# Performance work log

Measured on AMD Instinct MI355X. Metric: run time of the kernel, lower is better.

Reference implementation:

```python
import jax, jax.numpy as jnp
from jax import lax
import numpy as np

B, S = 128, 512
TARGET_SIZE = 32
T = TARGET_SIZE + 4  # tag_size, START = T-2, END = T-1


def setup_inputs() -> dict:
    key = jax.random.key(0)
    k1, k2, k3, k4 = jax.random.split(key, 4)
    feats = jax.random.normal(k1, (B, S, T), dtype=jnp.float32)
    # contiguous-prefix mask (lengths in [S//2, S])
    lengths = jax.random.randint(k2, (B,), S // 2, S + 1)
    mask = (jnp.arange(S)[None, :] < lengths[:, None]).astype(jnp.int32)
    tags = jax.random.randint(k3, (B, S), 0, TARGET_SIZE).astype(jnp.int32)
    # learned transitions, with the hard constraints from __init__
    transitions = 0.1 * jax.random.normal(k4, (T, T), dtype=jnp.float32)
    transitions = transitions.at[:, T - 2].set(-1000.0)  # nothing -> START
    transitions = transitions.at[T - 1, :].set(-1000.0)  # END -> nothing
    return {"feats": feats, "transitions": transitions, "mask": mask, "tags": tags}


def _nll(feats, transitions, mask, tags):
    # feats: (B,S,T), transitions: (T,T) with [i,j] = score(prev=i -> cur=j)
    b, s, t = feats.shape
    START, END = t - 2, t - 1
    fdtype = feats.dtype

    feats_t = jnp.swapaxes(feats, 0, 1)   # (S,B,T)
    mask_t = jnp.swapaxes(mask, 0, 1)     # (S,B)

    # ---- forward algorithm (partition function) ----
    # scores[t,b,i,j] = feats[b,t,j] + transitions[i,j]
    part0 = feats_t[0] + transitions[START][None, :]  # (B,T): alpha after step 0

    def step(part, xs):
        f_step, m_step = xs  # (B,T), (B,)
        # cur[b,i,j] = feats[b,j] + trans[i,j] + part[b,i]
        cur = f_step[:, None, :] + transitions[None, :, :] + part[:, :, None]
        new_part = jax.nn.logsumexp(cur, axis=1)  # (B,T)
        part = jnp.where(m_step[:, None].astype(bool), new_part, part)
        return part, None

    part, _ = lax.scan(step, part0, (feats_t[1:], mask_t[1:]))
    final = jax.nn.logsumexp(part[:, :, None] + transitions[None, :, :], axis=1)  # (B,T)
    forward_score = jnp.sum(final[:, END])

    # ---- gold score ----
    tags_i = tags.astype(jnp.int32)
    prev_tags = jnp.concatenate(
        [jnp.full((b, 1), START, dtype=jnp.int32), tags_i[:, :-1]], axis=1)  # (B,S)
    emit = jnp.take_along_axis(feats, tags_i[:, :, None], axis=2)[:, :, 0]    # (B,S)
    trans_sc = transitions[prev_tags, tags_i]                                  # (B,S)
    tg_energy = jnp.sum((emit + trans_sc) * mask.astype(fdtype))
    lengths = jnp.sum(mask, axis=1).astype(jnp.int32)                          # (B,)
    end_ids = jnp.take_along_axis(tags_i, (lengths - 1)[:, None], axis=1)[:, 0]
    end_energy = jnp.sum(transitions[end_ids, END])
    gold_score = tg_energy + end_energy

    # average_batch = True
    return (forward_score - gold_score) / jnp.asarray(b, fdtype)


def reference(feats, transitions, mask, tags):
    return _nll(feats, transitions, mask, tags)
```

## Files before the change

kernel.cpp:

```cpp
#include <hip/hip_runtime.h>


namespace {
constexpr int kB = 128;
constexpr int kS = 512;
constexpr int kT = 36;
constexpr int kStart = 34;
constexpr int kEnd = 35;

__device__ __forceinline__ float readlane_f(float v, int lane) {
    return __builtin_bit_cast(float, __builtin_amdgcn_readlane(__builtin_bit_cast(int, v), lane));
}

__device__ __forceinline__ float wave_sum(float v) {
#pragma unroll
    for (int off = 32; off; off >>= 1) v += __shfl_xor(v, off, 64);
    return v;
}

__device__ __forceinline__ int wave_sum_i(int v) {
#pragma unroll
    for (int off = 32; off; off >>= 1) v += __shfl_xor(v, off, 64);
    return v;
}

#define FOR36(X) \
    X(0, 0) X(1, 1) X(2, 2) X(3, 3) X(4, 0) X(5, 1) X(6, 2) X(7, 3) \
    X(8, 0) X(9, 1) X(10, 2) X(11, 3) X(12, 0) X(13, 1) X(14, 2) X(15, 3) \
    X(16, 0) X(17, 1) X(18, 2) X(19, 3) X(20, 0) X(21, 1) X(22, 2) X(23, 3) \
    X(24, 0) X(25, 1) X(26, 2) X(27, 3) X(28, 0) X(29, 1) X(30, 2) X(31, 3) \
    X(32, 0) X(33, 1) X(34, 2) X(35, 3)

#define FMDECL(n, a) float Fm##n;
#define FMINIT(n, a) Fm##n = __expf(trans[(n)*kT + jc]);
#define BMDECL(n, a) float Bm##n;
#define BMINIT(n, a) Bm##n = __expf(trans[jc * kT + (n)]);
#define FDOT(n, a) v##a = fmaf(readlane_f(q, n), Fm##n, v##a);
#define BDOT(n, a) w##a = fmaf(readlane_f(p, n), Bm##n, w##a);

#define LDF(t) fl[(size_t)(((t) < kS - 1) ? (t) : (kS - 1)) * kT]
#define LDBW(t) fl[(size_t)(((t) > 0) ? (t) : 0) * kT]

__global__ __attribute__((amdgpu_flat_work_group_size(128, 128),
                          amdgpu_waves_per_eu(1, 1)))
void crf_split_kernel(const float* __restrict__ feats,
                      const float* __restrict__ trans,
                      const int* __restrict__ mask,
                      const int* __restrict__ tags,
                      float* __restrict__ out) {
    const int b = blockIdx.x;
    const int tid = threadIdx.x;
    const int w = tid >> 6;
    const int j = tid & 63;
    const int jc = (j < kT) ? j : (kT - 1);
    const float* fbase = feats + (size_t)b * kS * kT;
    const float* fl = fbase + jc;
    const int* mb = mask + b * kS;
    const int* tb = tags + b * kS;

    __shared__ float gbuf[64];
    __shared__ float cbbuf;

    int len = 0;
#pragma unroll
    for (int k = 0; k < kS / 64; ++k) len += mb[k * 64 + j];
    len = wave_sum_i(len);

    float q = 0.f, Cf = 0.f;

    if (w == 1) {
        FOR36(BMDECL)
        FOR36(BMINIT)
        float g = (j < kT) ? __expf(trans[j * kT + kEnd]) : 0.f;
        float Cb = 0.f;

        auto bstep = [&](float eb, int tau) {
            const float p = eb * g;
            float w0 = 0.f, w1 = 0.f, w2 = 0.f, w3 = 0.f;
            FOR36(BDOT)
            const float ng = (w0 + w1) + (w2 + w3);
            g = (tau < len) ? ng : g;
        };
        auto renormB = [&]() {
            const float mg = readlane_f(g, 0);
            g *= __builtin_amdgcn_rcpf(mg);
            Cb += __logf(mg);
        };

        float pA0, pA1, pA2, pA3, pA4, pA5, pA6, pA7;
        float pB0, pB1, pB2, pB3, pB4, pB5, pB6, pB7;
        float eA0, eA1, eA2, eA3, eA4, eA5, eA6, eA7;
        pA0 = LDBW(511); pA1 = LDBW(510); pA2 = LDBW(509); pA3 = LDBW(508);
        pA4 = LDBW(507); pA5 = LDBW(506); pA6 = LDBW(505); pA7 = LDBW(504);
        eA0 = __expf(pA0); eA1 = __expf(pA1); eA2 = __expf(pA2); eA3 = __expf(pA3);
        eA4 = __expf(pA4); eA5 = __expf(pA5); eA6 = __expf(pA6); eA7 = __expf(pA7);

        int it0 = 0;
        while (it0 < kS / 2) {
            pB0 = LDBW(503 - it0); pB1 = LDBW(502 - it0); pB2 = LDBW(501 - it0); pB3 = LDBW(500 - it0);
            pB4 = LDBW(499 - it0); pB5 = LDBW(498 - it0); pB6 = LDBW(497 - it0); pB7 = LDBW(496 - it0);
            bstep(eA0, 511 - it0); bstep(eA1, 510 - it0);
            bstep(eA2, 509 - it0); bstep(eA3, 508 - it0);
            renormB();
            bstep(eA4, 507 - it0); bstep(eA5, 506 - it0);
            bstep(eA6, 505 - it0); bstep(eA7, 504 - it0);
            renormB();
            eA0 = __expf(pB0); eA1 = __expf(pB1); eA2 = __expf(pB2); eA3 = __expf(pB3);
            eA4 = __expf(pB4); eA5 = __expf(pB5); eA6 = __expf(pB6); eA7 = __expf(pB7);

            pA0 = LDBW(495 - it0); pA1 = LDBW(494 - it0); pA2 = LDBW(493 - it0); pA3 = LDBW(492 - it0);
            pA4 = LDBW(491 - it0); pA5 = LDBW(490 - it0); pA6 = LDBW(489 - it0); pA7 = LDBW(488 - it0);
            bstep(eA0, 503 - it0); bstep(eA1, 502 - it0);
            bstep(eA2, 501 - it0); bstep(eA3, 500 - it0);
            renormB();
            bstep(eA4, 499 - it0); bstep(eA5, 498 - it0);
            bstep(eA6, 497 - it0); bstep(eA7, 496 - it0);
            renormB();
            eA0 = __expf(pA0); eA1 = __expf(pA1); eA2 = __expf(pA2); eA3 = __expf(pA3);
            eA4 = __expf(pA4); eA5 = __expf(pA5); eA6 = __expf(pA6); eA7 = __expf(pA7);
            it0 += 16;
        }
        gbuf[j] = g;
        if (j == 0) cbbuf = Cb;
    } else {
        FOR36(FMDECL)
        FOR36(FMINIT)
        const float a0 = (j < kT) ? (fl[0] + trans[kStart * kT + jc]) : -1e30f;
        Cf = readlane_f(a0, 0);
        q = __expf(a0 - Cf);

        auto fstep = [&](float ef, int t) {
            float v0 = 0.f, v1 = 0.f, v2 = 0.f, v3 = 0.f;
            FOR36(FDOT)
            const float nq = ((v0 + v1) + (v2 + v3)) * ef;
            q = (t < kS / 2) ? nq : q;
        };
        auto renormF = [&]() {
            const float mf = readlane_f(q, 0);
            q *= __builtin_amdgcn_rcpf(mf);
            Cf += __logf(mf);
        };

        float pA0, pA1, pA2, pA3, pA4, pA5, pA6, pA7;
        float pB0, pB1, pB2, pB3, pB4, pB5, pB6, pB7;
        float eA0, eA1, eA2, eA3, eA4, eA5, eA6, eA7;
        pA0 = LDF(1); pA1 = LDF(2); pA2 = LDF(3); pA3 = LDF(4);
        pA4 = LDF(5); pA5 = LDF(6); pA6 = LDF(7); pA7 = LDF(8);
        eA0 = __expf(pA0); eA1 = __expf(pA1); eA2 = __expf(pA2); eA3 = __expf(pA3);
        eA4 = __expf(pA4); eA5 = __expf(pA5); eA6 = __expf(pA6); eA7 = __expf(pA7);

        int it0 = 0;
        while (it0 < kS / 2) {
            pB0 = LDF(it0 + 9);  pB1 = LDF(it0 + 10); pB2 = LDF(it0 + 11); pB3 = LDF(it0 + 12);
            pB4 = LDF(it0 + 13); pB5 = LDF(it0 + 14); pB6 = LDF(it0 + 15); pB7 = LDF(it0 + 16);
            fstep(eA0, it0 + 1); fstep(eA1, it0 + 2);
            fstep(eA2, it0 + 3); fstep(eA3, it0 + 4);
            renormF();
            fstep(eA4, it0 + 5); fstep(eA5, it0 + 6);
            fstep(eA6, it0 + 7); fstep(eA7, it0 + 8);
            renormF();
            eA0 = __expf(pB0); eA1 = __expf(pB1); eA2 = __expf(pB2); eA3 = __expf(pB3);
            eA4 = __expf(pB4); eA5 = __expf(pB5); eA6 = __expf(pB6); eA7 = __expf(pB7);

            pA0 = LDF(it0 + 17); pA1 = LDF(it0 + 18); pA2 = LDF(it0 + 19); pA3 = LDF(it0 + 20);
            pA4 = LDF(it0 + 21); pA5 = LDF(it0 + 22); pA6 = LDF(it0 + 23); pA7 = LDF(it0 + 24);
            fstep(eA0, it0 + 9);  fstep(eA1, it0 + 10);
            fstep(eA2, it0 + 11); fstep(eA3, it0 + 12);
            renormF();
            fstep(eA4, it0 + 13); fstep(eA5, it0 + 14);
            fstep(eA6, it0 + 15); fstep(eA7, it0 + 16);
            renormF();
            eA0 = __expf(pA0); eA1 = __expf(pA1); eA2 = __expf(pA2); eA3 = __expf(pA3);
            eA4 = __expf(pA4); eA5 = __expf(pA5); eA6 = __expf(pA6); eA7 = __expf(pA7);
            it0 += 16;
        }
    }

    __syncthreads();

    if (w == 0) {
        const float Z = wave_sum(q * gbuf[j]);
        const float forward_b = Cf + cbbuf + __logf(Z);

        float gold = 0.f;
        for (int k = j; k < kS; k += 64) {
            if (k < len) {
                const int tg = tb[k];
                const int pv = (k == 0) ? kStart : tb[k - 1];
                gold += fbase[(size_t)k * kT + tg] + trans[pv * kT + tg];
            }
        }
        gold = wave_sum(gold);

        if (j == 0) {
            gold += trans[tb[len - 1] * kT + kEnd];
            atomicAdd(out, (forward_b - gold) * (1.0f / kB));
        }
    }
}

}

extern "C" void kernel_launch(void* const* d_in, const int* in_sizes, int n_in,
                              void* d_out, int out_size, void* d_ws, size_t ws_size,
                              hipStream_t stream) {
    const float* feats = (const float*)d_in[0];
    const float* trans = (const float*)d_in[1];
    const int* mask = (const int*)d_in[2];
    const int* tags = (const int*)d_in[3];
    float* out = (float*)d_out;

    (void)hipMemsetAsync(out, 0, sizeof(float), stream);
    crf_split_kernel<<<dim3(kB), dim3(128), 0, stream>>>(feats, trans, mask, tags, out);
}
```

Measured before the change: 101.2 us.

## Split forward/backward CRF scans into separate single-wave blocks with meet kernel

The 128-thread block that ran the forward and backward half-scans as two waves becomes 256 single-wave blocks, one per batch item and direction. Each block writes its partial vector and log-scale to workspace, and a second kernel combines the halves and computes the gold score. The aim is to spread the serial scans over more CUs/SIMDs instead of pairing two waves per CU. The cost is an extra kernel launch and a round trip through global memory, and the gold-score work no longer overlaps the scan.

```diff
diff --git a/kernel.cpp b/kernel.cpp
--- a/kernel.cpp
+++ b/kernel.cpp
@@ -7,6 +7,7 @@
 constexpr int kT = 36;
 constexpr int kStart = 34;
 constexpr int kEnd = 35;
+constexpr int kWS = 144;
 
 __device__ __forceinline__ float readlane_f(float v, int lane) {
     return __builtin_bit_cast(float, __builtin_amdgcn_readlane(__builtin_bit_cast(int, v), lane));
@@ -41,34 +42,81 @@
 #define LDF(t) fl[(size_t)(((t) < kS - 1) ? (t) : (kS - 1)) * kT]
 #define LDBW(t) fl[(size_t)(((t) > 0) ? (t) : 0) * kT]
 
-__global__ __attribute__((amdgpu_flat_work_group_size(128, 128),
+
+__global__ __attribute__((amdgpu_flat_work_group_size(64, 64),
                           amdgpu_waves_per_eu(1, 1)))
-void crf_split_kernel(const float* __restrict__ feats,
-                      const float* __restrict__ trans,
-                      const int* __restrict__ mask,
-                      const int* __restrict__ tags,
-                      float* __restrict__ out) {
-    const int b = blockIdx.x;
-    const int tid = threadIdx.x;
-    const int w = tid >> 6;
-    const int j = tid & 63;
+void crf_scan_kernel(const float* __restrict__ feats,
+                     const float* __restrict__ trans,
+                     const int* __restrict__ mask,
+                     float* __restrict__ ws) {
+    const int b = blockIdx.x >> 1;
+    const int dir = blockIdx.x & 1;
+    const int j = threadIdx.x;
     const int jc = (j < kT) ? j : (kT - 1);
-    const float* fbase = feats + (size_t)b * kS * kT;
-    const float* fl = fbase + jc;
-    const int* mb = mask + b * kS;
-    const int* tb = tags + b * kS;
-
-    __shared__ float gbuf[64];
-    __shared__ float cbbuf;
-
-    int len = 0;
-#pragma unroll
-    for (int k = 0; k < kS / 64; ++k) len += mb[k * 64 + j];
-    len = wave_sum_i(len);
-
-    float q = 0.f, Cf = 0.f;
-
-    if (w == 1) {
+    const float* fl = feats + (size_t)b * kS * kT + jc;
+    float* wsb = ws + (size_t)b * kWS;
+
+    if (dir == 0) {
+        FOR36(FMDECL)
+        FOR36(FMINIT)
+        const float a0 = (j < kT) ? (fl[0] + trans[kStart * kT + jc]) : -1e30f;
+        float Cf = readlane_f(a0, 0);
+        float q = __expf(a0 - Cf);
+
+        auto fstep = [&](float ef, int t) {
+            float v0 = 0.f, v1 = 0.f, v2 = 0.f, v3 = 0.f;
+            FOR36(FDOT)
+            const float nq = ((v0 + v1) + (v2 + v3)) * ef;
+            q = (t < kS / 2) ? nq : q;
+        };
+        auto renormF = [&]() {
+            const float mf = readlane_f(q, 0);
+            q *= __builtin_amdgcn_rcpf(mf);
+            Cf += __logf(mf);
+        };
+
+        float pA0, pA1, pA2, pA3, pA4, pA5, pA6, pA7;
+        float pB0, pB1, pB2, pB3, pB4, pB5, pB6, pB7;
+        float eA0, eA1, eA2, eA3, eA4, eA5, eA6, eA7;
+        pA0 = LDF(1); pA1 = LDF(2); pA2 = LDF(3); pA3 = LDF(4);
+        pA4 = LDF(5); pA5 = LDF(6); pA6 = LDF(7); pA7 = LDF(8);
+        eA0 = __expf(pA0); eA1 = __expf(pA1); eA2 = __expf(pA2); eA3 = __expf(pA3);
+        eA4 = __expf(pA4); eA5 = __expf(pA5); eA6 = __expf(pA6); eA7 = __expf(pA7);
+
+        int it0 = 0;
+        while (it0 < kS / 2) {
+            pB0 = LDF(it0 + 9);  pB1 = LDF(it0 + 10); pB2 = LDF(it0 + 11); pB3 = LDF(it0 + 12);
+            pB4 = LDF(it0 + 13); pB5 = LDF(it0 + 14); pB6 = LDF(it0 + 15); pB7 = LDF(it0 + 16);
+            fstep(eA0, it0 + 1); fstep(eA1, it0 + 2);
+            fstep(eA2, it0 + 3); fstep(eA3, it0 + 4);
+            renormF();
+            fstep(eA4, it0 + 5); fstep(eA5, it0 + 6);
+            fstep(eA6, it0 + 7); fstep(eA7, it0 + 8);
+            renormF();
+            eA0 = __expf(pB0); eA1 = __expf(pB1); eA2 = __expf(pB2); eA3 = __expf(pB3);
+            eA4 = __expf(pB4); eA5 = __expf(pB5); eA6 = __expf(pB6); eA7 = __expf(pB7);
+
+            pA0 = LDF(it0 + 17); pA1 = LDF(it0 + 18); pA2 = LDF(it0 + 19); pA3 = LDF(it0 + 20);
+            pA4 = LDF(it0 + 21); pA5 = LDF(it0 + 22); pA6 = LDF(it0 + 23); pA7 = LDF(it0 + 24);
+            fstep(eA0, it0 + 9);  fstep(eA1, it0 + 10);
+            fstep(eA2, it0 + 11); fstep(eA3, it0 + 12);
+            renormF();
+            fstep(eA4, it0 + 13); fstep(eA5, it0 + 14);
+            fstep(eA6, it0 + 15); fstep(eA7, it0 + 16);
+            renormF();
+            eA0 = __expf(pA0); eA1 = __expf(pA1); eA2 = __expf(pA2); eA3 = __expf(pA3);
+            eA4 = __expf(pA4); eA5 = __expf(pA5); eA6 = __expf(pA6); eA7 = __expf(pA7);
+            it0 += 16;
+        }
+        wsb[j] = q;
+        if (j == 0) wsb[128] = Cf;
+    } else {
+        const int* mb = mask + b * kS;
+        int len = 0;
+#pragma unroll
+        for (int k = 0; k < kS / 64; ++k) len += mb[k * 64 + j];
+        len = wave_sum_i(len);
+
         FOR36(BMDECL)
         FOR36(BMINIT)
         float g = (j < kT) ? __expf(trans[j * kT + kEnd]) : 0.f;
@@ -120,82 +168,48 @@
             eA4 = __expf(pA4); eA5 = __expf(pA5); eA6 = __expf(pA6); eA7 = __expf(pA7);
             it0 += 16;
         }
-        gbuf[j] = g;
-        if (j == 0) cbbuf = Cb;
-    } else {
-        FOR36(FMDECL)
-        FOR36(FMINIT)
-        const float a0 = (j < kT) ? (fl[0] + trans[kStart * kT + jc]) : -1e30f;
-        Cf = readlane_f(a0, 0);
-        q = __expf(a0 - Cf);
-
-        auto fstep = [&](float ef, int t) {
-            float v0 = 0.f, v1 = 0.f, v2 = 0.f, v3 = 0.f;
-            FOR36(FDOT)
-            const float nq = ((v0 + v1) + (v2 + v3)) * ef;
-            q = (t < kS / 2) ? nq : q;
-        };
-        auto renormF = [&]() {
-            const float mf = readlane_f(q, 0);
-            q *= __builtin_amdgcn_rcpf(mf);
-            Cf += __logf(mf);
-        };
-
-        float pA0, pA1, pA2, pA3, pA4, pA5, pA6, pA7;
-        float pB0, pB1, pB2, pB3, pB4, pB5, pB6, pB7;
-        float eA0, eA1, eA2, eA3, eA4, eA5, eA6, eA7;
-        pA0 = LDF(1); pA1 = LDF(2); pA2 = LDF(3); pA3 = LDF(4);
-        pA4 = LDF(5); pA5 = LDF(6); pA6 = LDF(7); pA7 = LDF(8);
-        eA0 = __expf(pA0); eA1 = __expf(pA1); eA2 = __expf(pA2); eA3 = __expf(pA3);
-        eA4 = __expf(pA4); eA5 = __expf(pA5); eA6 = __expf(pA6); eA7 = __expf(pA7);
-
-        int it0 = 0;
-        while (it0 < kS / 2) {
-            pB0 = LDF(it0 + 9);  pB1 = LDF(it0 + 10); pB2 = LDF(it0 + 11); pB3 = LDF(it0 + 12);
-            pB4 = LDF(it0 + 13); pB5 = LDF(it0 + 14); pB6 = LDF(it0 + 15); pB7 = LDF(it0 + 16);
-            fstep(eA0, it0 + 1); fstep(eA1, it0 + 2);
-            fstep(eA2, it0 + 3); fstep(eA3, it0 + 4);
-            renormF();
-            fstep(eA4, it0 + 5); fstep(eA5, it0 + 6);
-            fstep(eA6, it0 + 7); fstep(eA7, it0 + 8);
-            renormF();
-            eA0 = __expf(pB0); eA1 = __expf(pB1); eA2 = __expf(pB2); eA3 = __expf(pB3);
-            eA4 = __expf(pB4); eA5 = __expf(pB5); eA6 = __expf(pB6); eA7 = __expf(pB7);
-
-            pA0 = LDF(it0 + 17); pA1 = LDF(it0 + 18); pA2 = LDF(it0 + 19); pA3 = LDF(it0 + 20);
-            pA4 = LDF(it0 + 21); pA5 = LDF(it0 + 22); pA6 = LDF(it0 + 23); pA7 = LDF(it0 + 24);
-            fstep(eA0, it0 + 9);  fstep(eA1, it0 + 10);
-            fstep(eA2, it0 + 11); fstep(eA3, it0 + 12);
-            renormF();
-            fstep(eA4, it0 + 13); fstep(eA5, it0 + 14);
-            fstep(eA6, it0 + 15); fstep(eA7, it0 + 16);
-            renormF();
-            eA0 = __expf(pA0); eA1 = __expf(pA1); eA2 = __expf(pA2); eA3 = __expf(pA3);
-            eA4 = __expf(pA4); eA5 = __expf(pA5); eA6 = __expf(pA6); eA7 = __expf(pA7);
-            it0 += 16;
+        wsb[64 + j] = g;
+        if (j == 0) wsb[129] = Cb;
+    }
+}
+
+
+__global__ __attribute__((amdgpu_flat_work_group_size(64, 64),
+                          amdgpu_waves_per_eu(1, 1)))
+void crf_meet_kernel(const float* __restrict__ feats,
+                     const float* __restrict__ trans,
+                     const int* __restrict__ mask,
+                     const int* __restrict__ tags,
+                     const float* __restrict__ ws,
+                     float* __restrict__ out) {
+    const int b = blockIdx.x;
+    const int j = threadIdx.x;
+    const float* fbase = feats + (size_t)b * kS * kT;
+    const int* mb = mask + b * kS;
+    const int* tb = tags + b * kS;
+    const float* wsb = ws + (size_t)b * kWS;
+
+    int len = 0;
+#pragma unroll
+    for (int k = 0; k < kS / 64; ++k) len += mb[k * 64 + j];
+    len = wave_sum_i(len);
+
+    const float Z = wave_sum(wsb[j] * wsb[64 + j]);
+    const float forward_b = wsb[128] + wsb[129] + __logf(Z);
+
+    float gold = 0.f;
+    for (int k = j; k < kS; k += 64) {
+        if (k < len) {
+            const int tg = tb[k];
+            const int pv = (k == 0) ? kStart : tb[k - 1];
+            gold += fbase[(size_t)k * kT + tg] + trans[pv * kT + tg];
         }
     }
-
-    __syncthreads();
-
-    if (w == 0) {
-        const float Z = wave_sum(q * gbuf[j]);
-        const float forward_b = Cf + cbbuf + __logf(Z);
-
-        float gold = 0.f;
-        for (int k = j; k < kS; k += 64) {
-            if (k < len) {
-                const int tg = tb[k];
-                const int pv = (k == 0) ? kStart : tb[k - 1];
-                gold += fbase[(size_t)k * kT + tg] + trans[pv * kT + tg];
-            }
-        }
-        gold = wave_sum(gold);
-
-        if (j == 0) {
-            gold += trans[tb[len - 1] * kT + kEnd];
-            atomicAdd(out, (forward_b - gold) * (1.0f / kB));
-        }
+    gold = wave_sum(gold);
+
+    if (j == 0) {
+        gold += trans[tb[len - 1] * kT + kEnd];
+        atomicAdd(out, (forward_b - gold) * (1.0f / kB));
     }
 }
 
@@ -209,7 +223,9 @@
     const int* mask = (const int*)d_in[2];
     const int* tags = (const int*)d_in[3];
     float* out = (float*)d_out;
+    float* ws = (float*)d_ws;
 
     (void)hipMemsetAsync(out, 0, sizeof(float), stream);
-    crf_split_kernel<<<dim3(kB), dim3(128), 0, stream>>>(feats, trans, mask, tags, out);
-}
+    crf_scan_kernel<<<dim3(2 * kB), dim3(64), 0, stream>>>(feats, trans, mask, ws);
+    crf_meet_kernel<<<dim3(kB), dim3(64), 0, stream>>>(feats, trans, mask, tags, ws, out);
+}
```

After: 107.0 us. 5.8% more time.
